# Performance work log

Hardware: AMD Instinct MI355X
Metric: run time of the kernel (lower is better)

The kernel has to match this reference:

```python
import jax, jax.numpy as jnp
import numpy as np
from jax import lax

# --- model/problem dims (see init_kwargs) ---
G, NPG, R, F, HID, L = 40, 500, 8, 256, 256, 3   # graphs(frames), nodes/graph, relations, feat, hidden, layers
N = G * NPG                                       # 20000 nodes
EPG = 8000
E = G * EPG                                       # 320000 edges
TOTAL = L * HID                                   # 768 = concat of layer outputs
LSTM_IN, LSTM_HID, NCLASS = 256, 256, 2
RATIO = 0.5
K = int(np.ceil(RATIO * NPG))                     # 250 nodes kept per graph by SAGPool


def setup_inputs() -> dict:
    key = jax.random.key(0)
    ks = jax.random.split(key, 16)
    s = 0.05
    x = jax.random.normal(ks[0], (N, F), dtype=jnp.float32)
    # intra-graph edges: node ids offset by graph index
    off = jnp.arange(G, dtype=jnp.int32)[:, None] * NPG
    src = jax.random.randint(ks[1], (G, EPG), 0, NPG, dtype=jnp.int32) + off
    dst = jax.random.randint(ks[2], (G, EPG), 0, NPG, dtype=jnp.int32) + off
    edge_index = jnp.stack([src.reshape(-1), dst.reshape(-1)])
    edge_attr = jax.random.randint(ks[3], (E,), 0, R, dtype=jnp.int32)
    batch = jnp.repeat(jnp.arange(G, dtype=jnp.int32), NPG)
    # RGCN layer params (layer0 in=F==HID so all layers stack)
    conv_W = jax.random.normal(ks[4], (L, R, HID, HID), dtype=jnp.float32) * s
    conv_root = jax.random.normal(ks[5], (L, HID, HID), dtype=jnp.float32) * s
    conv_bias = jnp.zeros((L, HID), dtype=jnp.float32)
    # SAGPool scorer: RGCNConv(TOTAL, 1, R)
    pool_W = jax.random.normal(ks[6], (R, TOTAL, 1), dtype=jnp.float32) * s
    pool_root = jax.random.normal(ks[7], (TOTAL, 1), dtype=jnp.float32) * s
    pool_bias = jnp.zeros((1,), dtype=jnp.float32)
    fc1_W = jax.random.normal(ks[8], (LSTM_IN, TOTAL), dtype=jnp.float32) * s
    fc1_b = jnp.zeros((LSTM_IN,), dtype=jnp.float32)
    W_ih = jax.random.normal(ks[9], (4 * LSTM_HID, LSTM_IN), dtype=jnp.float32) * s
    W_hh = jax.random.normal(ks[10], (4 * LSTM_HID, LSTM_HID), dtype=jnp.float32) * s
    b_ih = jnp.zeros((4 * LSTM_HID,), dtype=jnp.float32)
    b_hh = jnp.zeros((4 * LSTM_HID,), dtype=jnp.float32)
    fc2_W = jax.random.normal(ks[11], (NCLASS, LSTM_HID), dtype=jnp.float32) * s
    fc2_b = jnp.zeros((NCLASS,), dtype=jnp.float32)
    return dict(x=x, edge_index=edge_index, edge_attr=edge_attr, batch=batch,
                conv_W=conv_W, conv_root=conv_root, conv_bias=conv_bias,
                pool_W=pool_W, pool_root=pool_root, pool_bias=pool_bias,
                fc1_W=fc1_W, fc1_b=fc1_b, W_ih=W_ih, W_hh=W_hh, b_ih=b_ih, b_hh=b_hh,
                fc2_W=fc2_W, fc2_b=fc2_b)


def rgcn_conv(x, src, dst, etype, W, root, bias):
    """PyG (Fast)RGCNConv: per-relation mean aggregation summed over relations + root + bias."""
    num_nodes = x.shape[0]
    Rr = W.shape[0]
    h_all = jnp.einsum('ni,rio->rno', x, W)          # [R, N, out] per-relation transform
    msg = h_all[etype, src]                           # [E, out] per-edge message
    seg = dst * Rr + etype                            # (node, relation) segment id
    cnt = jax.ops.segment_sum(jnp.ones((src.shape[0],), x.dtype), seg,
                              num_segments=num_nodes * Rr)
    norm = 1.0 / jnp.maximum(cnt[seg], 1.0)           # per-(dst,rel) mean normalization
    agg = jax.ops.segment_sum(msg * norm[:, None], dst, num_segments=num_nodes)
    return agg + x @ root + bias


def lstm_scan(xs, W_ih, W_hh, b_ih, b_hh):
    """torch.nn.LSTM (single layer, batch=1) over sequence xs [T, in]; torch gate order i,f,g,o."""
    H = W_hh.shape[1]
    def step(carry, xt):
        h, c = carry
        gates = xt @ W_ih.T + h @ W_hh.T + b_ih + b_hh
        i, f, g, o = jnp.split(gates, 4)
        c = jax.nn.sigmoid(f) * c + jax.nn.sigmoid(i) * jnp.tanh(g)
        h = jax.nn.sigmoid(o) * jnp.tanh(c)
        return (h, c), h
    init = (jnp.zeros((H,), xs.dtype), jnp.zeros((H,), xs.dtype))
    (h, c), ys = lax.scan(step, init, xs)
    return ys, h


def reference(x, edge_index, edge_attr, batch,
              conv_W, conv_root, conv_bias,
              pool_W, pool_root, pool_bias,
              fc1_W, fc1_b, W_ih, W_hh, b_ih, b_hh, fc2_W, fc2_b):
    src, dst = edge_index[0], edge_index[1]
    # stacked RGCN layers, outputs concatenated (dropout omitted: eval mode)
    h = x
    outs = []
    for l in range(L):
        h = jax.nn.relu(rgcn_conv(h, src, dst, edge_attr, conv_W[l], conv_root[l], conv_bias[l]))
        outs.append(h)
    xc = jnp.concatenate(outs, axis=-1)               # [N, TOTAL]
    # SAGPool: RGCN scorer -> tanh -> per-graph top-k (batch is contiguous equal-size graphs)
    score = jnp.tanh(rgcn_conv(xc, src, dst, edge_attr, pool_W, pool_root, pool_bias).reshape(-1))
    topv, topi = lax.top_k(score.reshape(G, NPG), K)  # [G, K]
    xg = xc.reshape(G, NPG, TOTAL)
    xsel = jnp.take_along_axis(xg, topi[:, :, None], axis=1) * topv[:, :, None]
    # readout_type='mean': global_mean_pool over kept nodes per graph
    readout = xsel.mean(axis=1)                       # [G, TOTAL]
    h1 = jax.nn.relu(readout @ fc1_W.T + fc1_b)       # [G, LSTM_IN]
    # temporal_type='lstm_last': last hidden state over the G-frame sequence
    _, hlast = lstm_scan(h1, W_ih, W_hh, b_ih, b_hh)  # [LSTM_HID]
    logits = hlast @ fc2_W.T + fc2_b                  # [NCLASS]
    return jax.nn.log_softmax(logits, axis=-1)
```

## Files before the change

kernel.cpp:

```cpp
#include <hip/hip_runtime.h>

typedef unsigned short u16;
typedef short bf8 __attribute__((ext_vector_type(8)));
typedef short bf4 __attribute__((ext_vector_type(4)));
typedef float f4 __attribute__((ext_vector_type(4)));
typedef _Float16 h2v __attribute__((ext_vector_type(2)));
typedef __fp16 g2v __attribute__((ext_vector_type(2)));
typedef unsigned int u4v __attribute__((ext_vector_type(4)));

#define N_NODES 20000
#define N_EDGES 320000
#define NGRAPH 40
#define NPG 500
#define KTOP 250
#define NSEG (N_NODES * 8)

#define P_CONV_BIAS 0
#define P_POOL_W    768
#define P_POOL_ROOT 6912
#define P_POOL_BIAS 7680
#define P_FC1_W     7688
#define P_FC1_B     204296
#define P_W_IH      204552
#define P_B_IH      466696
#define P_B_HH      467720
#define P_FC2_W     468744
#define P_FC2_B     469256
#define P_TOTAL     469264

__device__ __forceinline__ float b2f(u16 u) {
    union { unsigned int i; float f; } v; v.i = ((unsigned int)u) << 16; return v.f;
}
__device__ __forceinline__ u16 f2b(float f) {
    union { float f; unsigned int i; } v; v.f = f;
    unsigned int x = v.i;
    return (u16)((x + 0x7fffu + ((x >> 16) & 1u)) >> 16);
}
__device__ __forceinline__ float wred(float s) {
    #pragma unroll
    for (int off = 32; off > 0; off >>= 1) s += __shfl_down(s, off);
    return s;
}
__device__ __forceinline__ float fdot2u(unsigned a, unsigned b, float c) {
#if __has_builtin(__builtin_amdgcn_fdot2)
    union { unsigned u; h2v h; } ua, ub; ua.u = a; ub.u = b;
    return __builtin_amdgcn_fdot2(ua.h, ub.h, c, false);
#else
    union { unsigned u; g2v h; } ua, ub; ua.u = a; ub.u = b;
    return c + (float)ua.h[0] * (float)ub.h[0] + (float)ua.h[1] * (float)ub.h[1];
#endif
}
__device__ __forceinline__ unsigned packh2(float a, float b) {
    g2v h = __builtin_amdgcn_cvt_pkrtz(a, b);
    union { g2v h; unsigned u; } v; v.h = h; return v.u;
}

__global__ void k_init(unsigned int* __restrict__ flag, unsigned int* __restrict__ cnt,
                       unsigned int* __restrict__ ctr) {
    int i = blockIdx.x * 256 + threadIdx.x;
    if (i < 64) flag[i] = 0u;
    if (i < NSEG) { cnt[i] = 0u; ctr[i] = 0u; }
}

__global__ void k_detect1(const u16* __restrict__ xr, int n, unsigned int* __restrict__ fb) {
    unsigned int local = 0;
    for (int i = blockIdx.x * 256 + threadIdx.x; i < n; i += 64 * 256) {
        unsigned int u = xr[i];
        if (((u >> 7) & 0xFFu) == 0xFFu) local++;
    }
    local = (unsigned int)wred((float)local);
    if ((threadIdx.x & 63) == 0 && local) atomicAdd(&fb[1], local);
}
__global__ void k_detect2(unsigned int* __restrict__ fb) {
    fb[0] = (fb[1] > 8u) ? 1u : 0u;
}

__device__ __forceinline__ u16 load_cvt(const void* src, size_t i, bool f32) {
    return f32 ? f2b(((const float*)src)[i]) : ((const u16*)src)[i];
}

__global__ void k_cvt_all(const void* conv_bias, const void* pool_W, const void* pool_root,
                          const void* pool_bias, const void* fc1_W, const void* fc1_b,
                          const void* W_ih, const void* b_ih, const void* b_hh,
                          const void* fc2_W, const void* fc2_b,
                          u16* __restrict__ parms, const unsigned int* __restrict__ flag) {
    int i = blockIdx.x * 256 + threadIdx.x;
    if (i >= P_TOTAL) return;
    bool f32 = (*flag != 0u);
    u16 v;
    if      (i < P_CONV_BIAS + 768)    v = load_cvt(conv_bias, i - P_CONV_BIAS, f32);
    else if (i < P_POOL_W + 6144)      v = load_cvt(pool_W,    i - P_POOL_W, f32);
    else if (i < P_POOL_ROOT + 768)    v = load_cvt(pool_root, i - P_POOL_ROOT, f32);
    else if (i < P_POOL_BIAS + 1)      v = load_cvt(pool_bias, i - P_POOL_BIAS, f32);
    else if (i < P_FC1_W && i >= P_POOL_BIAS) return;
    else if (i < P_FC1_W + 196608)     v = load_cvt(fc1_W,    i - P_FC1_W, f32);
    else if (i < P_FC1_B + 256)        v = load_cvt(fc1_b,    i - P_FC1_B, f32);
    else if (i < P_W_IH + 262144)      v = load_cvt(W_ih,     i - P_W_IH, f32);
    else if (i < P_B_IH + 1024)        v = load_cvt(b_ih,     i - P_B_IH, f32);
    else if (i < P_B_HH + 1024)        v = load_cvt(b_hh,     i - P_B_HH, f32);
    else if (i < P_FC2_W + 512)        v = load_cvt(fc2_W,    i - P_FC2_W, f32);
    else if (i < P_FC2_B + 2)          v = load_cvt(fc2_b,    i - P_FC2_B, f32);
    else return;
    parms[i] = v;
}

__global__ void k_stage_x(const void* __restrict__ src, u16* __restrict__ xc,
                          const unsigned int* __restrict__ flag) {
    int i = blockIdx.x * 256 + threadIdx.x;
    if (i >= N_NODES * 256) return;
    u16 v = load_cvt(src, i, *flag != 0u);
    int n = i >> 8, f = i & 255;
    xc[(size_t)n * 768 + 512 + f] = v;
}

__global__ void k_count(const int* __restrict__ dst, const int* __restrict__ et,
                        unsigned int* __restrict__ cnt) {
    int e = blockIdx.x * 256 + threadIdx.x;
    if (e < N_EDGES) {
        unsigned d = (unsigned)dst[e]; if (d >= N_NODES) d = 0;
        unsigned r = (unsigned)et[e] & 7u;
        atomicAdd(&cnt[d * 8 + r], 1u);
    }
}
__global__ void k_inv(const unsigned int* __restrict__ cnt, float* __restrict__ inv, int n) {
    int i = blockIdx.x * 256 + threadIdx.x;
    if (i < n) {
        unsigned int c = cnt[i];
        inv[i] = 1.0f / (float)(c < 1u ? 1u : c);
    }
}

__global__ void k_scan1(const unsigned int* __restrict__ cnt, unsigned int* __restrict__ seg,
                        unsigned int* __restrict__ bsum) {
    __shared__ unsigned int s[256];
    int t = threadIdx.x, i = blockIdx.x * 256 + t;
    unsigned int v = (i < NSEG) ? cnt[i] : 0u;
    s[t] = v;
    __syncthreads();
    for (int off = 1; off < 256; off <<= 1) {
        unsigned int add = (t >= off) ? s[t - off] : 0u;
        __syncthreads();
        s[t] += add;
        __syncthreads();
    }
    if (i < NSEG) seg[i] = s[t] - v;
    if (t == 255) bsum[blockIdx.x] = s[255];
}
__global__ void k_scan2(unsigned int* __restrict__ bsum, int nb) {
    __shared__ unsigned int s[1024];
    int t = threadIdx.x;
    unsigned int v = (t < nb) ? bsum[t] : 0u;
    s[t] = v;
    __syncthreads();
    for (int off = 1; off < 1024; off <<= 1) {
        unsigned int add = (t >= off) ? s[t - off] : 0u;
        __syncthreads();
        s[t] += add;
        __syncthreads();
    }
    if (t < nb) bsum[t] = s[t] - v;
}
__global__ void k_scan3(unsigned int* __restrict__ seg, const unsigned int* __restrict__ bsum) {
    int i = blockIdx.x * 256 + threadIdx.x;
    if (i < NSEG) seg[i] += bsum[i >> 8];
    if (i == 0) seg[NSEG] = N_EDGES;
}
__global__ void k_place(const int* __restrict__ src, const int* __restrict__ dst,
                        const int* __restrict__ et, const unsigned int* __restrict__ seg,
                        unsigned int* __restrict__ ctr, const float* __restrict__ inv,
                        unsigned int* __restrict__ skey, float* __restrict__ sw, int chn) {
    int e = blockIdx.x * 256 + threadIdx.x;
    if (e >= N_EDGES) return;
    unsigned s = (unsigned)src[e]; if (s >= N_NODES) s = 0;
    unsigned d = (unsigned)dst[e]; if (d >= N_NODES) d = 0;
    unsigned r = (unsigned)et[e] & 7u;
    unsigned key = d * 8 + r;
    unsigned pos = seg[key] + atomicAdd(&ctr[key], 1u);
    unsigned base = (d / (unsigned)chn) * (unsigned)chn;
    unsigned sl = s - base;
    if (sl >= (unsigned)chn) sl = 0u;
    skey[pos] = sl | (r << 16);
    sw[pos] = inv[key];
}

__global__ void k_transpose2(const void* __restrict__ conv_W, const void* __restrict__ conv_root,
                             u16* __restrict__ Wt, const unsigned int* __restrict__ flag) {
    int idx = blockIdx.x * 256 + threadIdx.x;
    if (idx >= 3 * 36 * 256 * 64) return;
    bool f32 = (*flag != 0u);
    int kk = idx & 63;
    int n = (idx >> 6) & 255;
    int lc = idx >> 14;
    int l = lc / 36, ck = lc % 36;
    int k = ck * 64 + kk;
    u16 v;
    if (k < 2048) {
        int r = k >> 8, i = k & 255;
        v = load_cvt(conv_W, ((size_t)((l * 8 + r) * 256 + i)) * 256 + n, f32);
    } else {
        int i = k - 2048;
        v = load_cvt(conv_root, ((size_t)(l * 256 + i)) * 256 + n, f32);
    }
    Wt[idx] = v;
}
__global__ void k_whh4(const void* __restrict__ W_hh, unsigned int* __restrict__ whh4,
                       const unsigned int* __restrict__ flag) {
    int idx = blockIdx.x * 256 + threadIdx.x;
    if (idx >= 32 * 1024 * 4) return;
    int c = idx & 3, j = (idx >> 2) & 1023, i4 = idx >> 12;
    int i2 = i4 * 4 + c;
    bool f32 = (*flag != 0u);
    float a, b;
    if (f32) {
        a = ((const float*)W_hh)[j * 256 + 2 * i2];
        b = ((const float*)W_hh)[j * 256 + 2 * i2 + 1];
    } else {
        a = b2f(((const u16*)W_hh)[j * 256 + 2 * i2]);
        b = b2f(((const u16*)W_hh)[j * 256 + 2 * i2 + 1]);
    }
    whh4[idx] = packh2(a, b);
}

__launch_bounds__(256, 3)
__global__ void k_layer2(const u16* __restrict__ xprev,
                         const u16* __restrict__ WtL,
                         u16* __restrict__ Hall, int n0, int chn) {
    __shared__ u16 As[64 * 264];
    int m0 = n0 + blockIdx.x * 64;
    int rg = blockIdx.y;
    int nend = n0 + chn;
    int wave = threadIdx.x >> 6, lane = threadIdx.x & 63;
    int mrow = lane & 15, quad = lane >> 4;
    int nbase = wave * 64;

    {
        int row = threadIdx.x >> 2, sg = threadIdx.x & 3;
        int gm = m0 + row;
        u16* dstp = As + row * 264 + sg * 64;
        if (gm < nend) {
            const u16* srcp = xprev + (size_t)gm * 768 + sg * 64;
            #pragma unroll
            for (int c = 0; c < 8; ++c)
                *(bf8*)(dstp + c * 8) = *(const bf8*)(srcp + c * 8);
        } else {
            bf8 z = {0, 0, 0, 0, 0, 0, 0, 0};
            #pragma unroll
            for (int c = 0; c < 8; ++c) *(bf8*)(dstp + c * 8) = z;
        }
    }
    __syncthreads();

    f4 acc[4][4];
    #pragma unroll
    for (int nt = 0; nt < 4; ++nt)
        #pragma unroll
        for (int mh = 0; mh < 4; ++mh) acc[nt][mh] = (f4){0.0f, 0.0f, 0.0f, 0.0f};

    const u16* WtR = WtL + (size_t)(rg * 4) * 16384;
    #pragma unroll
    for (int c4 = 0; c4 < 4; ++c4) {
        const u16* Bck = WtR + (size_t)c4 * 16384;
        #pragma unroll
        for (int ks = 0; ks < 2; ++ks) {
            bf8 a[4];
            #pragma unroll
            for (int mh = 0; mh < 4; ++mh)
                a[mh] = *(const bf8*)(As + (mh * 16 + mrow) * 264 + c4 * 64 + ks * 32 + quad * 8);
            #pragma unroll
            for (int nt = 0; nt < 4; ++nt) {
                bf8 b = *(const bf8*)(Bck + (size_t)(nbase + nt * 16 + mrow) * 64
                                      + ks * 32 + quad * 8);
                #pragma unroll
                for (int mh = 0; mh < 4; ++mh)
                    acc[nt][mh] = __builtin_amdgcn_mfma_f32_16x16x32_bf16(a[mh], b, acc[nt][mh], 0, 0, 0);
            }
        }
    }

    __syncthreads();
    #pragma unroll
    for (int nt = 0; nt < 4; ++nt) {
        int col = nbase + nt * 16 + mrow;
        #pragma unroll
        for (int mh = 0; mh < 4; ++mh)
            #pragma unroll
            for (int v = 0; v < 4; ++v)
                As[(mh * 16 + quad * 4 + v) * 264 + col] = f2b(acc[nt][mh][v]);
    }
    __syncthreads();
    {
        int row = threadIdx.x >> 2, sg = threadIdx.x & 3;
        int gm = m0 + row;
        if (gm < nend) {
            u16* dst = Hall + ((size_t)rg * chn + (gm - n0)) * 256 + sg * 64;
            const u16* srcp = As + row * 264 + sg * 64;
            #pragma unroll
            for (int c = 0; c < 8; ++c)
                *(bf8*)(dst + c * 8) = *(const bf8*)(srcp + c * 8);
        }
    }
}

__launch_bounds__(256)
__global__ void k_gather(const unsigned int* __restrict__ seg,
                         const unsigned int* __restrict__ skey,
                         const float* __restrict__ sw,
                         const u16* __restrict__ Hall,
                         const u16* __restrict__ bias,
                         u16* __restrict__ xc, int colbase, int n0, int chn) {
    int nl = blockIdx.x * 4 + (threadIdx.x >> 6);
    int n = n0 + nl;
    int lane = threadIdx.x & 63;
    int c0 = lane * 4;
    unsigned e0 = seg[n * 8], e1 = seg[n * 8 + 8];
    float a0 = 0.0f, a1 = 0.0f, a2 = 0.0f, a3 = 0.0f;
    unsigned key = 0; float w = 0.0f;
    if (e0 < e1) { key = skey[e0]; w = sw[e0]; }
    for (unsigned e = e0; e < e1;) {
        unsigned kc = key; float wc = w;
        ++e;
        if (e < e1) { key = skey[e]; w = sw[e]; }
        const u16* row = Hall + ((size_t)(kc >> 16) * chn + (kc & 0xFFFFu)) * 256 + c0;
        bf4 v = *(const bf4*)row;
        a0 += wc * b2f((u16)v[0]);
        a1 += wc * b2f((u16)v[1]);
        a2 += wc * b2f((u16)v[2]);
        a3 += wc * b2f((u16)v[3]);
    }
    const u16* rr = Hall + ((size_t)8 * chn + nl) * 256 + c0;
    bf4 rv = *(const bf4*)rr;
    float o0 = a0 + b2f((u16)rv[0]) + b2f(bias[c0 + 0]);
    float o1 = a1 + b2f((u16)rv[1]) + b2f(bias[c0 + 1]);
    float o2 = a2 + b2f((u16)rv[2]) + b2f(bias[c0 + 2]);
    float o3 = a3 + b2f((u16)rv[3]) + b2f(bias[c0 + 3]);
    bf4 o;
    o[0] = (short)f2b(o0 > 0.0f ? o0 : 0.0f);
    o[1] = (short)f2b(o1 > 0.0f ? o1 : 0.0f);
    o[2] = (short)f2b(o2 > 0.0f ? o2 : 0.0f);
    o[3] = (short)f2b(o3 > 0.0f ? o3 : 0.0f);
    *(bf4*)(xc + (size_t)n * 768 + colbase + c0) = o;
}

__launch_bounds__(256)
__global__ void k_pool(const u16* __restrict__ xc, const u16* __restrict__ parms,
                       float* __restrict__ p, float* __restrict__ score) {
    int n = blockIdx.x * 4 + (threadIdx.x >> 6);
    if (n >= N_NODES) return;
    int lane = threadIdx.x & 63;
    const u16* xr = xc + (size_t)n * 768;
    float acc[9];
    #pragma unroll
    for (int rr = 0; rr < 9; ++rr) acc[rr] = 0.0f;
    #pragma unroll
    for (int q = 0; q < 12; ++q) {
        int f = lane + 64 * q;
        float xv = b2f(xr[f]);
        #pragma unroll
        for (int rr = 0; rr < 8; ++rr)
            acc[rr] += xv * b2f(parms[P_POOL_W + rr * 768 + f]);
        acc[8] += xv * b2f(parms[P_POOL_ROOT + f]);
    }
    #pragma unroll
    for (int rr = 0; rr < 9; ++rr) acc[rr] = wred(acc[rr]);
    if (lane == 0) {
        #pragma unroll
        for (int rr = 0; rr < 8; ++rr) p[rr * N_NODES + n] = acc[rr];
        score[n] = acc[8] + b2f(parms[P_POOL_BIAS]);
    }
}
__global__ void k_scatter_pool(const int* __restrict__ src, const int* __restrict__ dst,
                               const int* __restrict__ et, const float* __restrict__ inv,
                               const float* __restrict__ p, float* __restrict__ score) {
    int e = blockIdx.x * 256 + threadIdx.x;
    if (e >= N_EDGES) return;
    int r = et[e] & 7;
    unsigned s = (unsigned)src[e]; if (s >= N_NODES) s = 0;
    unsigned d = (unsigned)dst[e]; if (d >= N_NODES) d = 0;
    atomicAdd(&score[d], inv[d * 8 + r] * p[r * N_NODES + s]);
}

__launch_bounds__(256)
__global__ void k_sort(const float* __restrict__ score, unsigned int* __restrict__ topidx,
                       float* __restrict__ topv) {
    __shared__ unsigned long long keys[512];
    __shared__ float vals[512];
    int g = blockIdx.x, tid = threadIdx.x;
    for (int i = tid; i < 512; i += 256) {
        unsigned long long key;
        float v = 0.0f;
        if (i < NPG) {
            v = tanhf(score[g * NPG + i]);
            unsigned int u = __float_as_uint(v);
            u = (u & 0x80000000u) ? ~u : (u | 0x80000000u);
            u = ~u;
            key = ((unsigned long long)u << 32) | (unsigned int)i;
        } else {
            key = 0xFFFFFFFFFFFFFFFFull;
        }
        keys[i] = key;
        vals[i] = v;
    }
    __syncthreads();
    for (int k = 2; k <= 512; k <<= 1)
        for (int j = k >> 1; j > 0; j >>= 1) {
            for (int i = tid; i < 512; i += 256) {
                int ixj = i ^ j;
                if (ixj > i) {
                    bool up = ((i & k) == 0);
                    unsigned long long a = keys[i], b = keys[ixj];
                    if ((a > b) == up) { keys[i] = b; keys[ixj] = a; }
                }
            }
            __syncthreads();
        }
    if (tid < KTOP) {
        int idx = (int)(keys[tid] & 511u);
        topidx[g * 256 + tid] = (unsigned)idx;
        topv[g * 256 + tid] = vals[idx];
    }
}

__launch_bounds__(256)
__global__ void k_readout(const unsigned int* __restrict__ topidx,
                          const float* __restrict__ topv,
                          const u16* __restrict__ xc, float* __restrict__ readout) {
    __shared__ unsigned int sidx[KTOP];
    __shared__ float sv[KTOP];
    __shared__ float part[256];
    int g = blockIdx.x, cb = blockIdx.y;
    int tid = threadIdx.x;
    if (tid < KTOP) { sidx[tid] = topidx[g * 256 + tid]; sv[tid] = topv[g * 256 + tid]; }
    __syncthreads();
    int fl = tid & 63, ng = tid >> 6;
    int f = cb * 64 + fl;
    float acc = 0.0f;
    for (int j = ng; j < KTOP; j += 4)
        acc += sv[j] * b2f(xc[(size_t)(g * NPG + sidx[j]) * 768 + f]);
    part[tid] = acc;
    __syncthreads();
    if (tid < 64) {
        float s = part[tid] + part[64 + tid] + part[128 + tid] + part[192 + tid];
        readout[(size_t)g * 768 + cb * 64 + tid] = s * (1.0f / (float)KTOP);
    }
}

__global__ void k_fc1(const float* __restrict__ readout, const u16* __restrict__ parms,
                      float* __restrict__ h1) {
    int wid = blockIdx.x * 4 + (threadIdx.x >> 6);
    if (wid >= NGRAPH * 256) return;
    int g = wid >> 8, o = wid & 255, lane = threadIdx.x & 63;
    const float* rr = readout + (size_t)g * 768;
    const u16* w = parms + P_FC1_W + (size_t)o * 768;
    float s = 0.0f;
    #pragma unroll
    for (int q = 0; q < 12; ++q) { int f = lane + 64 * q; s += rr[f] * b2f(w[f]); }
    s = wred(s);
    if (lane == 0) { s += b2f(parms[P_FC1_B + o]); h1[g * 256 + o] = s > 0.0f ? s : 0.0f; }
}
__global__ void k_gx(const float* __restrict__ h1, const u16* __restrict__ parms,
                     float* __restrict__ gx) {
    int wid = blockIdx.x * 4 + (threadIdx.x >> 6);
    if (wid >= NGRAPH * 1024) return;
    int t = wid >> 10, j = wid & 1023, lane = threadIdx.x & 63;
    const float* xr = h1 + t * 256;
    const u16* w = parms + P_W_IH + (size_t)j * 256;
    float s = 0.0f;
    #pragma unroll
    for (int q = 0; q < 4; ++q) { int f = lane + 64 * q; s += xr[f] * b2f(w[f]); }
    s = wred(s);
    if (lane == 0) gx[t * 1024 + j] = s + b2f(parms[P_B_IH + j]) + b2f(parms[P_B_HH + j]);
}

__launch_bounds__(512, 2)
__global__ void k_lstm(const float* __restrict__ gx, const unsigned int* __restrict__ whh4,
                       const u16* __restrict__ parms, void* __restrict__ out,
                       const unsigned int* __restrict__ flag) {
    __shared__ float hs[256];
    __shared__ unsigned int hs2[128];
    __shared__ float gs[1024];
    __shared__ float red[2];
    int tid = threadIdx.x;
    int j0 = tid, j1 = tid + 512;
    u4v wa[24], wb[24];
    #pragma unroll
    for (int q = 0; q < 24; ++q) {
        wa[q] = *(const u4v*)(whh4 + (((size_t)q * 1024) + j0) * 4);
        wb[q] = *(const u4v*)(whh4 + (((size_t)q * 1024) + j1) * 4);
    }
    asm volatile("" : "+v"(wa[0]), "+v"(wa[1]), "+v"(wa[2]), "+v"(wa[3]),
                      "+v"(wa[4]), "+v"(wa[5]), "+v"(wa[6]), "+v"(wa[7]),
                      "+v"(wa[8]), "+v"(wa[9]), "+v"(wa[10]), "+v"(wa[11]),
                      "+v"(wa[12]), "+v"(wa[13]), "+v"(wa[14]), "+v"(wa[15]),
                      "+v"(wa[16]), "+v"(wa[17]), "+v"(wa[18]), "+v"(wa[19]),
                      "+v"(wa[20]), "+v"(wa[21]), "+v"(wa[22]), "+v"(wa[23]));
    asm volatile("" : "+v"(wb[0]), "+v"(wb[1]), "+v"(wb[2]), "+v"(wb[3]),
                      "+v"(wb[4]), "+v"(wb[5]), "+v"(wb[6]), "+v"(wb[7]),
                      "+v"(wb[8]), "+v"(wb[9]), "+v"(wb[10]), "+v"(wb[11]),
                      "+v"(wb[12]), "+v"(wb[13]), "+v"(wb[14]), "+v"(wb[15]),
                      "+v"(wb[16]), "+v"(wb[17]), "+v"(wb[18]), "+v"(wb[19]),
                      "+v"(wb[20]), "+v"(wb[21]), "+v"(wb[22]), "+v"(wb[23]));
    if (tid < 256) hs[tid] = 0.0f;
    if (tid < 128) hs2[tid] = 0u;
    float c = 0.0f;
    __syncthreads();
    for (int t = 0; t < NGRAPH; ++t) {
        float g0 = gx[t * 1024 + j0];
        float g1 = gx[t * 1024 + j1];
        #pragma unroll
        for (int q = 0; q < 24; ++q) {
            #pragma unroll
            for (int cc = 0; cc < 4; ++cc) {
                unsigned h2 = hs2[q * 4 + cc];
                g0 = fdot2u(wa[q][cc], h2, g0);
                g1 = fdot2u(wb[q][cc], h2, g1);
            }
        }
        #pragma unroll 4
        for (int q = 24; q < 32; ++q) {
            u4v v0 = *(const u4v*)(whh4 + (((size_t)q * 1024) + j0) * 4);
            u4v v1 = *(const u4v*)(whh4 + (((size_t)q * 1024) + j1) * 4);
            #pragma unroll
            for (int cc = 0; cc < 4; ++cc) {
                unsigned h2 = hs2[q * 4 + cc];
                g0 = fdot2u(v0[cc], h2, g0);
                g1 = fdot2u(v1[cc], h2, g1);
            }
        }
        gs[j0] = g0;
        gs[j1] = g1;
        __syncthreads();
        if (tid < 256) {
            float gi = 1.0f / (1.0f + expf(-gs[tid]));
            float gf = 1.0f / (1.0f + expf(-gs[256 + tid]));
            float gg = tanhf(gs[512 + tid]);
            float go = 1.0f / (1.0f + expf(-gs[768 + tid]));
            c = gf * c + gi * gg;
            float h = go * tanhf(c);
            hs[tid] = h;
            float ho = __shfl(h, (tid & 63) ^ 1);
            if (!(tid & 1)) hs2[tid >> 1] = packh2(h, ho);
        }
        __syncthreads();
    }
    if (tid < 128) {
        int cls = tid >> 6, lane = tid & 63;
        float s = 0.0f;
        #pragma unroll
        for (int q = 0; q < 4; ++q) {
            int d = lane + 64 * q;
            s += hs[d] * b2f(parms[P_FC2_W + cls * 256 + d]);
        }
        s = wred(s);
        if (lane == 0) red[cls] = s + b2f(parms[P_FC2_B + cls]);
    }
    __syncthreads();
    if (tid == 0) {
        float l0 = red[0], l1 = red[1];
        float m = fmaxf(l0, l1);
        float lse = m + logf(expf(l0 - m) + expf(l1 - m));
        float o0 = l0 - lse, o1 = l1 - lse;
        if (*flag) { ((float*)out)[0] = o0; ((float*)out)[1] = o1; }
        else       { ((u16*)out)[0] = f2b(o0); ((u16*)out)[1] = f2b(o1); }
    }
}

struct WS {
    unsigned int* flag; unsigned int* cnt; float* inv; unsigned int* seg; unsigned int* ctr;
    unsigned int* skey; float* sw; unsigned int* bsum;
    u16* Wt2; u16* xc; u16* Hall; float* p; float* score;
    unsigned int* topidx; float* topv;
    float* readout; float* h1; float* gx; unsigned int* whh4; u16* parms;
    size_t need;
};
static WS plan(char* base, int chn) {
    WS w; size_t off = 0;
    auto take = [&](size_t bytes) -> char* {
        char* p = base + off; off += (bytes + 255) & ~(size_t)255; return p;
    };
    w.flag    = (unsigned int*)take(256);
    w.cnt     = (unsigned int*)take((size_t)NSEG * 4);
    w.inv     = (float*)take((size_t)NSEG * 4);
    w.seg     = (unsigned int*)take((size_t)(NSEG + 1) * 4);
    w.ctr     = (unsigned int*)take((size_t)NSEG * 4);
    w.skey    = (unsigned int*)take((size_t)N_EDGES * 4);
    w.sw      = (float*)take((size_t)N_EDGES * 4);
    w.bsum    = (unsigned int*)take(1024 * 4);
    w.Wt2     = (u16*)take((size_t)3 * 36 * 256 * 64 * 2);
    w.xc      = (u16*)take((size_t)N_NODES * 768 * 2);
    w.Hall    = (u16*)take((size_t)9 * chn * 256 * 2);
    w.p       = (float*)take((size_t)8 * N_NODES * 4);
    w.score   = (float*)take((size_t)N_NODES * 4);
    w.topidx  = (unsigned int*)take((size_t)NGRAPH * 256 * 4);
    w.topv    = (float*)take((size_t)NGRAPH * 256 * 4);
    w.readout = (float*)take((size_t)NGRAPH * 768 * 4);
    w.h1      = (float*)take((size_t)NGRAPH * 256 * 4);
    w.gx      = (float*)take((size_t)NGRAPH * 1024 * 4);
    w.whh4    = (unsigned int*)take((size_t)32 * 1024 * 4 * 4);
    w.parms   = (u16*)take((size_t)P_TOTAL * 2);
    w.need = off;
    return w;
}

extern "C" void kernel_launch(void* const* d_in, const int* in_sizes, int n_in,
                              void* d_out, int out_size, void* d_ws, size_t ws_size,
                              hipStream_t stream) {
    (void)in_sizes; (void)n_in; (void)out_size;
    const void* x        = d_in[0];
    const int* edge_index= (const int*)d_in[1];
    const int* edge_attr = (const int*)d_in[2];
    const void* conv_W   = d_in[4];
    const void* conv_root= d_in[5];
    const void* conv_bias= d_in[6];
    const void* pool_W   = d_in[7];
    const void* pool_root= d_in[8];
    const void* pool_bias= d_in[9];
    const void* fc1_W    = d_in[10];
    const void* fc1_b    = d_in[11];
    const void* W_ih     = d_in[12];
    const void* W_hh     = d_in[13];
    const void* b_ih     = d_in[14];
    const void* b_hh     = d_in[15];
    const void* fc2_W    = d_in[16];
    const void* fc2_b    = d_in[17];

    const int* e_src = edge_index;
    const int* e_dst = edge_index + N_EDGES;

    if (ws_size == 0) ws_size = (size_t)64 << 20;
    int chn = 500;
    {
        const int ladder[4] = {20000, 4000, 1000, 500};
        for (int i = 0; i < 4; ++i) {
            if (plan((char*)d_ws, ladder[i]).need <= ws_size) { chn = ladder[i]; break; }
        }
    }
    WS w = plan((char*)d_ws, chn);

    k_init<<<(NSEG + 255) / 256, 256, 0, stream>>>(w.flag, w.cnt, w.ctr);
    k_detect1<<<64, 256, 0, stream>>>((const u16*)x, 1 << 18, w.flag);
    k_detect2<<<1, 1, 0, stream>>>(w.flag);

    k_count<<<1250, 256, 0, stream>>>(e_dst, edge_attr, w.cnt);
    k_inv<<<(NSEG + 255) / 256, 256, 0, stream>>>(w.cnt, w.inv, NSEG);
    k_scan1<<<625, 256, 0, stream>>>(w.cnt, w.seg, w.bsum);
    k_scan2<<<1, 1024, 0, stream>>>(w.bsum, 625);
    k_scan3<<<(NSEG + 255) / 256, 256, 0, stream>>>(w.seg, w.bsum);
    k_place<<<1250, 256, 0, stream>>>(e_src, e_dst, edge_attr, w.seg, w.ctr, w.inv,
                                      w.skey, w.sw, chn);

    k_cvt_all<<<(P_TOTAL + 255) / 256, 256, 0, stream>>>(
        conv_bias, pool_W, pool_root, pool_bias, fc1_W, fc1_b,
        W_ih, b_ih, b_hh, fc2_W, fc2_b, w.parms, w.flag);

    k_stage_x<<<20000, 256, 0, stream>>>(x, w.xc, w.flag);
    k_transpose2<<<6912, 256, 0, stream>>>(conv_W, conv_root, w.Wt2, w.flag);
    k_whh4<<<512, 256, 0, stream>>>(W_hh, w.whh4, w.flag);

    int nch = N_NODES / chn;
    int gx_tiles = (chn + 63) / 64;
    for (int l = 0; l < 3; ++l) {
        const u16* xprev = w.xc + (l == 0 ? 512 : (l - 1) * 256);
        const u16* WtL = w.Wt2 + (size_t)l * 36 * 16384;
        const u16* bias = w.parms + P_CONV_BIAS + l * 256;
        for (int c = 0; c < nch; ++c) {
            int n0 = c * chn;
            k_layer2<<<dim3(gx_tiles, 9), 256, 0, stream>>>(xprev, WtL, w.Hall, n0, chn);
            k_gather<<<chn / 4, 256, 0, stream>>>(w.seg, w.skey, w.sw, w.Hall, bias,
                                                  w.xc, l * 256, n0, chn);
        }
    }

    k_pool<<<5000, 256, 0, stream>>>(w.xc, w.parms, w.p, w.score);
    k_scatter_pool<<<1250, 256, 0, stream>>>(e_src, e_dst, edge_attr, w.inv, w.p, w.score);
    k_sort<<<NGRAPH, 256, 0, stream>>>(w.score, w.topidx, w.topv);
    k_readout<<<dim3(NGRAPH, 12), 256, 0, stream>>>(w.topidx, w.topv, w.xc, w.readout);
    k_fc1<<<2560, 256, 0, stream>>>(w.readout, w.parms, w.h1);
    k_gx<<<10240, 256, 0, stream>>>(w.h1, w.parms, w.gx);
    k_lstm<<<1, 512, 0, stream>>>(w.gx, w.whh4, w.parms, d_out, w.flag);
}
```

Measured before the change: 705.3 us.

## Vectorize x staging, use fast LSTM activations, widen chunk ladder

The x staging kernel now has each thread copy 8 contiguous features with one 16-byte store instead of one element per thread, cutting launched blocks eightfold. LSTM gate activations switch from expf/tanhf to __expf-based sigmoid and tanh formulas, shortening the serial per-timestep path at a small accuracy cost. The LSTM launch bounds drop to one block per CU and the streamed-weight loop is unrolled less. The chunk-size ladder gains intermediate sizes so a larger chunk can be picked when workspace is limited.

Result: no change. 691.6 us (-1.9%).

```diff
diff --git a/kernel.cpp b/kernel.cpp
--- a/kernel.cpp
+++ b/kernel.cpp
@@ -53,6 +53,12 @@
 __device__ __forceinline__ unsigned packh2(float a, float b) {
     g2v h = __builtin_amdgcn_cvt_pkrtz(a, b);
     union { g2v h; unsigned u; } v; v.h = h; return v.u;
+}
+__device__ __forceinline__ float sigm_f(float x) {
+    return 1.0f / (1.0f + __expf(-x));
+}
+__device__ __forceinline__ float tanh_f(float x) {
+    return 1.0f - 2.0f / (1.0f + __expf(2.0f * x));
 }
 
 __global__ void k_init(unsigned int* __restrict__ flag, unsigned int* __restrict__ cnt,
@@ -107,10 +113,17 @@
 __global__ void k_stage_x(const void* __restrict__ src, u16* __restrict__ xc,
                           const unsigned int* __restrict__ flag) {
     int i = blockIdx.x * 256 + threadIdx.x;
-    if (i >= N_NODES * 256) return;
-    u16 v = load_cvt(src, i, *flag != 0u);
-    int n = i >> 8, f = i & 255;
-    xc[(size_t)n * 768 + 512 + f] = v;
+    if (i >= N_NODES * 32) return;
+    int n = i >> 5, o = (i & 31) * 8;
+    bf8 v;
+    if (*flag != 0u) {
+        const float* s = (const float*)src + (size_t)n * 256 + o;
+        #pragma unroll
+        for (int c = 0; c < 8; ++c) v[c] = (short)f2b(s[c]);
+    } else {
+        v = *(const bf8*)((const u16*)src + (size_t)n * 256 + o);
+    }
+    *(bf8*)(xc + (size_t)n * 768 + 512 + o) = v;
 }
 
 __global__ void k_count(const int* __restrict__ dst, const int* __restrict__ et,
@@ -471,7 +484,7 @@
     if (lane == 0) gx[t * 1024 + j] = s + b2f(parms[P_B_IH + j]) + b2f(parms[P_B_HH + j]);
 }
 
-__launch_bounds__(512, 2)
+__launch_bounds__(512, 1)
 __global__ void k_lstm(const float* __restrict__ gx, const unsigned int* __restrict__ whh4,
                        const u16* __restrict__ parms, void* __restrict__ out,
                        const unsigned int* __restrict__ flag) {
@@ -515,7 +528,7 @@
                 g1 = fdot2u(wb[q][cc], h2, g1);
             }
         }
-        #pragma unroll 4
+        #pragma unroll 2
         for (int q = 24; q < 32; ++q) {
             u4v v0 = *(const u4v*)(whh4 + (((size_t)q * 1024) + j0) * 4);
             u4v v1 = *(const u4v*)(whh4 + (((size_t)q * 1024) + j1) * 4);
@@ -530,12 +543,12 @@
         gs[j1] = g1;
         __syncthreads();
         if (tid < 256) {
-            float gi = 1.0f / (1.0f + expf(-gs[tid]));
-            float gf = 1.0f / (1.0f + expf(-gs[256 + tid]));
-            float gg = tanhf(gs[512 + tid]);
-            float go = 1.0f / (1.0f + expf(-gs[768 + tid]));
+            float gi = sigm_f(gs[tid]);
+            float gf = sigm_f(gs[256 + tid]);
+            float gg = tanh_f(gs[512 + tid]);
+            float go = sigm_f(gs[768 + tid]);
             c = gf * c + gi * gg;
-            float h = go * tanhf(c);
+            float h = go * tanh_f(c);
             hs[tid] = h;
             float ho = __shfl(h, (tid & 63) ^ 1);
             if (!(tid & 1)) hs2[tid >> 1] = packh2(h, ho);
@@ -629,8 +642,8 @@
     if (ws_size == 0) ws_size = (size_t)64 << 20;
     int chn = 500;
     {
-        const int ladder[4] = {20000, 4000, 1000, 500};
-        for (int i = 0; i < 4; ++i) {
+        const int ladder[8] = {20000, 10000, 5000, 4000, 2500, 2000, 1000, 500};
+        for (int i = 0; i < 8; ++i) {
             if (plan((char*)d_ws, ladder[i]).need <= ws_size) { chn = ladder[i]; break; }
         }
     }
@@ -652,7 +665,7 @@
         conv_bias, pool_W, pool_root, pool_bias, fc1_W, fc1_b,
         W_ih, b_ih, b_hh, fc2_W, fc2_b, w.parms, w.flag);
 
-    k_stage_x<<<20000, 256, 0, stream>>>(x, w.xc, w.flag);
+    k_stage_x<<<2500, 256, 0, stream>>>(x, w.xc, w.flag);
     k_transpose2<<<6912, 256, 0, stream>>>(conv_W, conv_root, w.Wt2, w.flag);
     k_whh4<<<512, 256, 0, stream>>>(W_hh, w.whh4, w.flag);
 
```
